# Optimization experiments

Hardware: AMD Instinct MI355X
Metric: run time of the kernel (lower is better)

The kernel has to match this reference:

```python
import jax, jax.numpy as jnp
import numpy as np
import math

MAX_SEQ_LEN = 10000
WINDOW = 7
CANTOR_MAX_DEPTH = 8
DRAGON_MAX_ITERS = 10


def _cantor_indices(seq_len):
    depth = min(int(math.log2(seq_len)), CANTOR_MAX_DEPTH - 1)
    positions = [0.0, 1.0]
    for _ in range(depth):
        new = []
        for i in range(len(positions) - 1):
            l, r = positions[i], positions[i + 1]
            third = (r - l) / 3
            new.extend([l, l + third])
        new.append(positions[-1])
        positions = new
    idx = (np.array(positions) * (seq_len - 1)).astype(np.int64)
    return np.unique(idx)


def _dragon_weights(seq_len):
    iterations = min(int(math.log2(seq_len)), DRAGON_MAX_ITERS - 1)
    pattern = [0.5]
    for _ in range(iterations):
        pattern = pattern + [0.5] + [1.0 - x for x in reversed(pattern)]
    p = np.asarray(pattern, dtype=np.float32)
    p = (p - p.min()) / (p.max() - p.min() + 1e-8)
    if len(p) == seq_len:
        return p
    x_old = np.linspace(0.0, 1.0, len(p)).astype(np.float32)
    x_new = np.linspace(0.0, 1.0, seq_len).astype(np.float32)
    idx = np.searchsorted(x_old, x_new)
    lo = np.clip(idx - 1, 0, len(p) - 1)
    hi = np.clip(idx, 0, len(p) - 1)
    alpha = (x_new - x_old[lo]) / (x_old[hi] - x_old[lo] + 1e-8)
    w = (1.0 - alpha) * p[lo] + alpha * p[hi]
    w = np.where(idx == 0, p[0], w)
    w = np.where(idx >= len(p), p[-1], w)
    return w.astype(np.float32)


def _d2xy(n, d):
    x = y = 0
    s = 1
    while s < n:
        rx = 1 & (d // 2)
        ry = 1 & (d ^ rx)
        if ry == 0:
            if rx == 1:
                x, y = s - 1 - x, s - 1 - y
            x, y = y, x
        x += s * rx
        y += s * ry
        d //= 4
        s *= 2
    return x, y


def _xy2d(n, x, y):
    d = 0
    s = n // 2
    while s > 0:
        rx = 1 if x & s > 0 else 0
        ry = 1 if y & s > 0 else 0
        d += s * s * ((3 * rx) ^ ry)
        if ry == 0:
            if rx == 1:
                x, y = s - 1 - x, s - 1 - y
            x, y = y, x
        s //= 2
    return d


def _hilbert_local_indices(center_idx, seq_len):
    order = int(math.ceil(math.log2(math.sqrt(MAX_SEQ_LEN))))
    grid = 2 ** order
    n_coords = min(MAX_SEQ_LEN, grid * grid)
    center_idx = min(center_idx, n_coords - 1)
    cx, cy = _d2xy(grid, center_idx)
    half = WINDOW // 2
    idxs = []
    for dx in range(-half, half + 1):
        for dy in range(-half, half + 1):
            x, y = cx + dx, cy + dy
            if 0 <= x < grid and 0 <= y < grid:
                i = _xy2d(grid, int(x), int(y))
                if i < seq_len:
                    idxs.append(i)
    return np.asarray(idxs, dtype=np.int64)


def _attend(q, k, v, scale):
    # q: (B,1,H), k/v: (B,S,H) -> (B,H)
    scores = jnp.einsum('bqh,bkh->bqk', q, k) * scale
    attn = jax.nn.softmax(scores, axis=-1)
    return jnp.einsum('bqk,bkh->bqh', attn, v)[:, 0, :]


def setup_inputs() -> dict:
    key = jax.random.key(0)
    k1, k2, k3, k4 = jax.random.split(key, 4)
    B, L, H = 8, 8192, 1024
    return {
        'query': jax.random.normal(k1, (B, 1, H), dtype=jnp.float32),
        'key': jax.random.normal(k2, (B, L, H), dtype=jnp.float32),
        'value': jax.random.normal(k3, (B, L, H), dtype=jnp.float32),
        'pattern_weights': jax.random.uniform(k4, (3,), dtype=jnp.float32),
        'query_idx': 1234,
    }


def reference(query, key, value, pattern_weights, query_idx):
    B, L, H = key.shape
    scale = 1.0 / math.sqrt(query.shape[-1])

    # Hilbert local-window attention
    local_idx = jnp.asarray(_hilbert_local_indices(int(query_idx), L))
    hilbert_out = _attend(query, key[:, local_idx, :], value[:, local_idx, :], scale)

    # Cantor-set sparse global attention
    cantor_idx = jnp.asarray(_cantor_indices(L))
    cantor_out = _attend(query, key[:, cantor_idx, :], value[:, cantor_idx, :], scale)

    # Dragon-curve weighted full attention
    dw = jnp.asarray(_dragon_weights(L))  # (L,)
    dragon_out = _attend(query, key * dw[None, :, None], value, scale)

    w = jax.nn.softmax(pattern_weights, axis=0)
    return w[0] * hilbert_out + w[1] * cantor_out + w[2] * dragon_out
```

## Files before the change

kernel.cpp:

```cpp
#include <hip/hip_runtime.h>
#include <math.h>

#define B 8
#define L 8192
#define H 1024
#define SCALE 0.03125f

#define MAX_N 160
#define KP    128
#define ROWS  (L / KP)

#define OFF_OUTS 0
#define OFF_PART (OFF_OUTS + 2 * B * H)

__device__ inline void d2xy_dev(int n, int d, int* px, int* py) {
    int x = 0, y = 0;
    for (int s = 1; s < n; s *= 2) {
        int rx = 1 & (d / 2);
        int ry = 1 & (d ^ rx);
        if (ry == 0) {
            if (rx == 1) { x = s - 1 - x; y = s - 1 - y; }
            int t = x; x = y; y = t;
        }
        x += s * rx; y += s * ry;
        d /= 4;
    }
    *px = x; *py = y;
}

__device__ inline int xy2d_dev(int n, int x, int y) {
    int d = 0;
    for (int s = n / 2; s > 0; s /= 2) {
        int rx = ((x & s) > 0) ? 1 : 0;
        int ry = ((y & s) > 0) ? 1 : 0;
        d += s * s * ((3 * rx) ^ ry);
        if (ry == 0) {
            if (rx == 1) { x = s - 1 - x; y = s - 1 - y; }
            int t = x; x = y; y = t;
        }
    }
    return d;
}

__global__ __launch_bounds__(1024)
void mega_kernel(const float* __restrict__ q, const float* __restrict__ k,
                 const float* __restrict__ v, const int* __restrict__ qidx_p,
                 float* __restrict__ ws_f) {
    int bid = blockIdx.x;
    int tid = threadIdx.x;

    if (bid < 16) {
        int set = bid >> 3;
        int b   = bid & 7;

        __shared__ float qs[H];
        __shared__ float sc[MAX_N];
        __shared__ float probs[MAX_N];
        __shared__ int   idx[MAX_N];
        __shared__ int   n_sh;
        __shared__ float sinv_sh;

        if (tid < H / 4)
            ((float4*)qs)[tid] = ((const float4*)(q + (size_t)b * H))[tid];

        if (set == 1) {
            if (tid < 129) {
                double l = (tid == 128) ? 1.0 : 0.0;
                if (tid < 128) {
                    double gap = 1.0;
                    #pragma unroll
                    for (int bit = 6; bit >= 0; --bit) {
                        double third = gap / 3.0;
                        if ((tid >> bit) & 1) { l += third; gap -= third; }
                        else                  { gap = third; }
                    }
                }
                idx[tid] = (int)(l * (double)(L - 1));
            }
            if (tid == 0) n_sh = 129;
        } else {
            if (tid < 64) {
                int center = qidx_p[0];
                if (center > 9999) center = 9999;
                if (center < 0) center = 0;
                int cx, cy;
                d2xy_dev(128, center, &cx, &cy);
                int val = -1;
                if (tid < 49) {
                    int x = cx + tid / 7 - 3, y = cy + tid % 7 - 3;
                    if (x >= 0 && x < 128 && y >= 0 && y < 128) {
                        int i = xy2d_dev(128, x, y);
                        if (i < L) val = i;
                    }
                }
                unsigned long long ball = __ballot(val >= 0);
                int pos = __popcll(ball & ((1ull << tid) - 1));
                if (val >= 0) idx[pos] = val;
                if (tid == 0) n_sh = __popcll(ball);
            }
        }
        __syncthreads();
        int n = n_sh;

        int wid = tid >> 6, lane = tid & 63;
        for (int j = wid; j < n; j += 16) {
            const float4* k4 =
                (const float4*)(k + ((size_t)b * L + (size_t)idx[j]) * H);
            float p = 0.f;
            #pragma unroll
            for (int i = 0; i < H / 256; i++) {
                float4 a = ((float4*)qs)[lane + i * 64];
                float4 c = k4[lane + i * 64];
                p += a.x * c.x + a.y * c.y + a.z * c.z + a.w * c.w;
            }
            #pragma unroll
            for (int off = 32; off; off >>= 1) p += __shfl_down(p, off);
            if (lane == 0) sc[j] = p * SCALE;
        }
        __syncthreads();

        if (wid == 0) {
            float m = -1e30f;
            for (int j = lane; j < n; j += 64) m = fmaxf(m, sc[j]);
            #pragma unroll
            for (int mask = 32; mask; mask >>= 1) m = fmaxf(m, __shfl_xor(m, mask));
            float s = 0.f;
            for (int j = lane; j < n; j += 64) {
                float e = expf(sc[j] - m);
                probs[j] = e;
                s += e;
            }
            #pragma unroll
            for (int mask = 32; mask; mask >>= 1) s += __shfl_xor(s, mask);
            if (lane == 0) sinv_sh = 1.f / s;
        }
        __syncthreads();

        float acc = 0.f;
        float sinv = sinv_sh;
        #pragma unroll 4
        for (int j = 0; j < n; j++)
            acc += probs[j] * v[((size_t)b * L + (size_t)idx[j]) * H + tid];
        ws_f[OFF_OUTS + ((size_t)set * B + b) * H + tid] = acc * sinv;

    } else {
        int cb = bid - 16;
        int kp = cb >> 3, b = cb & 7;
        int c  = tid & 255;
        int r4 = tid >> 8;

        const float4* base =
            (const float4*)(v + ((size_t)b * L + (size_t)kp * ROWS) * H);
        float4 acc = make_float4(0.f, 0.f, 0.f, 0.f);
        for (int rr = r4; rr < ROWS; rr += 4) {
            float4 x = base[(size_t)rr * (H / 4) + c];
            acc.x += x.x; acc.y += x.y; acc.z += x.z; acc.w += x.w;
        }

        __shared__ float4 red[4][256];
        red[r4][c] = acc;
        __syncthreads();
        if (r4 == 0) {
            float4 a0 = red[0][c], a1 = red[1][c], a2 = red[2][c], a3 = red[3][c];
            float4 s = make_float4(a0.x + a1.x + a2.x + a3.x,
                                   a0.y + a1.y + a2.y + a3.y,
                                   a0.z + a1.z + a2.z + a3.z,
                                   a0.w + a1.w + a2.w + a3.w);
            ((float4*)(ws_f + OFF_PART + ((size_t)kp * B + b) * H))[c] = s;
        }
    }
}

__global__ __launch_bounds__(256)
void combine_kernel(const float* __restrict__ pw, const float* __restrict__ ws_f,
                    float* __restrict__ out) {
    int i = blockIdx.x * 256 + threadIdx.x;
    if (i >= B * H) return;
    float w0 = pw[0], w1 = pw[1], w2 = pw[2];
    float m  = fmaxf(w0, fmaxf(w1, w2));
    float e0 = expf(w0 - m), e1 = expf(w1 - m), e2 = expf(w2 - m);
    float invs = 1.f / (e0 + e1 + e2);

    const float* hil = ws_f + OFF_OUTS;
    const float* can = hil + B * H;
    const float* partials = ws_f + OFF_PART;

    float s = 0.f;
    #pragma unroll 8
    for (int kp = 0; kp < KP; kp++) s += partials[(size_t)kp * B * H + i];
    float mean = s * (1.0f / (float)L);

    out[i] = (e0 * hil[i] + e1 * can[i] + e2 * mean) * invs;
}

extern "C" void kernel_launch(void* const* d_in, const int* in_sizes, int n_in,
                              void* d_out, int out_size, void* d_ws, size_t ws_size,
                              hipStream_t stream) {
    const float* q  = (const float*)d_in[0];
    const float* k  = (const float*)d_in[1];
    const float* v  = (const float*)d_in[2];
    const float* pw = (const float*)d_in[3];
    const int* qidx = (const int*)d_in[4];

    float* ws_f = (float*)d_ws;

    mega_kernel<<<16 + KP * B, 1024, 0, stream>>>(q, k, v, qidx, ws_f);
    combine_kernel<<<(B * H + 255) / 256, 256, 0, stream>>>(pw, ws_f,
                                                            (float*)d_out);
}
```

Measured before the change: 62.01 us.

## Fuse combine into main kernel via last-block atomic counter and resize blocks

Removes the separate combine kernel. Each block bumps a per-batch atomic counter, and the last block to finish for a batch reduces the partial column sums and writes the final output. Blocks shrink to 512 threads and the mean pass uses 64 chunks per batch, writing two partials per block instead of reducing through shared memory. The sparse-attention value pass switches to float2 loads. This adds a memset launch and a serial tail reduction over 128 partials in one block per batch.

New measurement: 112.0 us. +80.7%, slower.

```diff
diff --git a/kernel.cpp b/kernel.cpp
--- a/kernel.cpp
+++ b/kernel.cpp
@@ -7,11 +7,13 @@
 #define SCALE 0.03125f
 
 #define MAX_N 160
-#define KP    128
-#define ROWS  (L / KP)
+#define KPB   64
+#define ROWSC (L / KPB)
+#define NPART (2 * KPB)
 
 #define OFF_OUTS 0
-#define OFF_PART (OFF_OUTS + 2 * B * H)
+#define OFF_PART (2 * B * H)
+#define OFF_CNT  (OFF_PART + NPART * B * H)
 
 __device__ inline void d2xy_dev(int n, int d, int* px, int* py) {
     int x = 0, y = 0;
@@ -42,16 +44,20 @@
     return d;
 }
 
-__global__ __launch_bounds__(1024)
+__global__ __launch_bounds__(512)
 void mega_kernel(const float* __restrict__ q, const float* __restrict__ k,
                  const float* __restrict__ v, const int* __restrict__ qidx_p,
-                 float* __restrict__ ws_f) {
+                 const float* __restrict__ pw, float* __restrict__ ws_f,
+                 int* __restrict__ cnt, float* __restrict__ out) {
     int bid = blockIdx.x;
     int tid = threadIdx.x;
+    int myb;
+    __shared__ int last_sh;
 
     if (bid < 16) {
         int set = bid >> 3;
         int b   = bid & 7;
+        myb = b;
 
         __shared__ float qs[H];
         __shared__ float sc[MAX_N];
@@ -103,7 +109,7 @@
         int n = n_sh;
 
         int wid = tid >> 6, lane = tid & 63;
-        for (int j = wid; j < n; j += 16) {
+        for (int j = wid; j < n; j += 8) {
             const float4* k4 =
                 (const float4*)(k + ((size_t)b * L + (size_t)idx[j]) * H);
             float p = 0.f;
@@ -136,61 +142,71 @@
         }
         __syncthreads();
 
-        float acc = 0.f;
+        float ax = 0.f, ay = 0.f;
+        #pragma unroll 4
+        for (int j = 0; j < n; j++) {
+            float p = probs[j];
+            const float2 x =
+                *(const float2*)(v + ((size_t)b * L + (size_t)idx[j]) * H + 2 * tid);
+            ax += p * x.x; ay += p * x.y;
+        }
         float sinv = sinv_sh;
-        #pragma unroll 4
-        for (int j = 0; j < n; j++)
-            acc += probs[j] * v[((size_t)b * L + (size_t)idx[j]) * H + tid];
-        ws_f[OFF_OUTS + ((size_t)set * B + b) * H + tid] = acc * sinv;
+        ((float2*)(ws_f + OFF_OUTS + ((size_t)set * B + b) * H))[tid] =
+            make_float2(ax * sinv, ay * sinv);
 
     } else {
         int cb = bid - 16;
         int kp = cb >> 3, b = cb & 7;
-        int c  = tid & 255;
-        int r4 = tid >> 8;
+        myb = b;
+        int c4 = tid & 255;
+        int r2 = tid >> 8;
 
         const float4* base =
-            (const float4*)(v + ((size_t)b * L + (size_t)kp * ROWS) * H);
+            (const float4*)(v + ((size_t)b * L + (size_t)kp * ROWSC) * H);
         float4 acc = make_float4(0.f, 0.f, 0.f, 0.f);
-        for (int rr = r4; rr < ROWS; rr += 4) {
-            float4 x = base[(size_t)rr * (H / 4) + c];
+        #pragma unroll 4
+        for (int rr = r2; rr < ROWSC; rr += 2) {
+            float4 x = base[(size_t)rr * (H / 4) + c4];
             acc.x += x.x; acc.y += x.y; acc.z += x.z; acc.w += x.w;
         }
-
-        __shared__ float4 red[4][256];
-        red[r4][c] = acc;
-        __syncthreads();
-        if (r4 == 0) {
-            float4 a0 = red[0][c], a1 = red[1][c], a2 = red[2][c], a3 = red[3][c];
-            float4 s = make_float4(a0.x + a1.x + a2.x + a3.x,
-                                   a0.y + a1.y + a2.y + a3.y,
-                                   a0.z + a1.z + a2.z + a3.z,
-                                   a0.w + a1.w + a2.w + a3.w);
-            ((float4*)(ws_f + OFF_PART + ((size_t)kp * B + b) * H))[c] = s;
-        }
-    }
-}
-
-__global__ __launch_bounds__(256)
-void combine_kernel(const float* __restrict__ pw, const float* __restrict__ ws_f,
-                    float* __restrict__ out) {
-    int i = blockIdx.x * 256 + threadIdx.x;
-    if (i >= B * H) return;
-    float w0 = pw[0], w1 = pw[1], w2 = pw[2];
-    float m  = fmaxf(w0, fmaxf(w1, w2));
-    float e0 = expf(w0 - m), e1 = expf(w1 - m), e2 = expf(w2 - m);
-    float invs = 1.f / (e0 + e1 + e2);
-
-    const float* hil = ws_f + OFF_OUTS;
-    const float* can = hil + B * H;
-    const float* partials = ws_f + OFF_PART;
-
-    float s = 0.f;
-    #pragma unroll 8
-    for (int kp = 0; kp < KP; kp++) s += partials[(size_t)kp * B * H + i];
-    float mean = s * (1.0f / (float)L);
-
-    out[i] = (e0 * hil[i] + e1 * can[i] + e2 * mean) * invs;
+        ((float4*)(ws_f + OFF_PART + (((size_t)(kp * 2 + r2)) * B + b) * H))[c4] = acc;
+    }
+
+    __syncthreads();
+    if (tid == 0) {
+        __threadfence();
+        int old = __hip_atomic_fetch_add(&cnt[myb], 1, __ATOMIC_ACQ_REL,
+                                         __HIP_MEMORY_SCOPE_AGENT);
+        last_sh = (old == KPB + 2 - 1);
+    }
+    __syncthreads();
+    if (last_sh) {
+        __threadfence();
+        if (tid < 256) {
+            float w0 = pw[0], w1 = pw[1], w2 = pw[2];
+            float m  = fmaxf(w0, fmaxf(w1, w2));
+            float e0 = expf(w0 - m), e1 = expf(w1 - m), e2 = expf(w2 - m);
+            float invs = 1.f / (e0 + e1 + e2);
+            int b = myb;
+
+            float4 s = make_float4(0.f, 0.f, 0.f, 0.f);
+            for (int p2 = 0; p2 < NPART; p2++) {
+                float4 x = ((const float4*)(ws_f + OFF_PART +
+                                            ((size_t)p2 * B + b) * H))[tid];
+                s.x += x.x; s.y += x.y; s.z += x.z; s.w += x.w;
+            }
+            float4 hil = ((const float4*)(ws_f + OFF_OUTS + (size_t)b * H))[tid];
+            float4 can = ((const float4*)(ws_f + OFF_OUTS +
+                                          ((size_t)B + b) * H))[tid];
+            const float il = 1.0f / (float)L;
+            float4 o;
+            o.x = (e0 * hil.x + e1 * can.x + e2 * (s.x * il)) * invs;
+            o.y = (e0 * hil.y + e1 * can.y + e2 * (s.y * il)) * invs;
+            o.z = (e0 * hil.z + e1 * can.z + e2 * (s.z * il)) * invs;
+            o.w = (e0 * hil.w + e1 * can.w + e2 * (s.w * il)) * invs;
+            ((float4*)(out + (size_t)b * H))[tid] = o;
+        }
+    }
 }
 
 extern "C" void kernel_launch(void* const* d_in, const int* in_sizes, int n_in,
@@ -203,8 +219,9 @@
     const int* qidx = (const int*)d_in[4];
 
     float* ws_f = (float*)d_ws;
-
-    mega_kernel<<<16 + KP * B, 1024, 0, stream>>>(q, k, v, qidx, ws_f);
-    combine_kernel<<<(B * H + 255) / 256, 256, 0, stream>>>(pw, ws_f,
-                                                            (float*)d_out);
-}
+    int*   cnt  = (int*)((char*)d_ws + (size_t)OFF_CNT * 4);
+
+    hipMemsetAsync(cnt, 0, B * sizeof(int), stream);
+    mega_kernel<<<16 + KPB * B, 512, 0, stream>>>(q, k, v, qidx, pw, ws_f, cnt,
+                                                  (float*)d_out);
+}
```
